# Kernel optimization log

Hardware: AMD Instinct MI355X
Metric: run time of the kernel (lower is better)

Reference implementation:

```python
import jax, jax.numpy as jnp
import numpy as np

EPS = 1e-6

def _rms_norm(x, w):
    # RMSNorm over last dim (head_dim)
    var = jnp.mean(jnp.square(x), axis=-1, keepdims=True)
    return x * jax.lax.rsqrt(var + EPS) * w

def _apply_rope(x, cos, sin):
    # x: [b, s, h, d]; cos/sin: [s, d]. Interleaved (real, imag) pairs as in
    # diffusers apply_rotary_emb (use_real_unbind_dim=-1) used by Flux.
    xr = x[..., 0::2]
    xi = x[..., 1::2]
    rotated = jnp.stack([-xi, xr], axis=-1).reshape(x.shape)
    cs = cos[None, :, None, :]
    sn = sin[None, :, None, :]
    return x * cs + rotated * sn

def setup_inputs() -> dict:
    key = jax.random.key(0)
    ks = jax.random.split(key, 10)
    b, s, dim, h, hd = 1, 2048, 3072, 24, 128
    inner = h * hd
    scale = 1.0 / np.sqrt(dim)
    x = jax.random.normal(ks[0], (b, s, dim), dtype=jnp.float32)
    # rope tables: proper cos/sin of log-spaced frequencies
    pos = jnp.arange(s, dtype=jnp.float32)[:, None]
    freqs = 1.0 / (10000.0 ** (jnp.arange(0, hd, 2, dtype=jnp.float32) / hd))
    angles = pos * freqs[None, :]                      # [s, hd/2]
    angles = jnp.repeat(angles, 2, axis=-1)            # [s, hd] interleaved pairs
    rope_cos = jnp.cos(angles)
    rope_sin = jnp.sin(angles)
    Wq = jax.random.normal(ks[1], (dim, inner), dtype=jnp.float32) * scale
    Wk = jax.random.normal(ks[2], (dim, inner), dtype=jnp.float32) * scale
    Wv = jax.random.normal(ks[3], (dim, inner), dtype=jnp.float32) * scale
    bq = jax.random.normal(ks[4], (inner,), dtype=jnp.float32) * 0.01
    bk = jax.random.normal(ks[5], (inner,), dtype=jnp.float32) * 0.01
    bv = jax.random.normal(ks[6], (inner,), dtype=jnp.float32) * 0.01
    gq = jnp.ones((hd,), dtype=jnp.float32)
    gk = jnp.ones((hd,), dtype=jnp.float32)
    return {"x": x, "rope_cos": rope_cos, "rope_sin": rope_sin,
            "Wq": Wq, "bq": bq, "Wk": Wk, "bk": bk, "Wv": Wv, "bv": bv,
            "gq": gq, "gk": gk}

def reference(x, rope_cos, rope_sin, Wq, bq, Wk, bk, Wv, bv, gq, gk):
    b, s, _ = x.shape
    h, hd = 24, 128
    q = (x @ Wq + bq).reshape(b, s, h, hd)
    k = (x @ Wk + bk).reshape(b, s, h, hd)
    v = (x @ Wv + bv).reshape(b, s, h, hd)
    q = _apply_rope(_rms_norm(q, gq), rope_cos, rope_sin)
    k = _apply_rope(_rms_norm(k, gk), rope_cos, rope_sin)
    scale = 1.0 / jnp.sqrt(jnp.asarray(hd, dtype=q.dtype))
    scores = jnp.einsum('bshd,bthd->bhst', q, k) * scale
    attn = jax.nn.softmax(scores, axis=-1)
    out = jnp.einsum('bhst,bthd->bshd', attn, v)
    return out.reshape(b, s, h * hd)
```

## Files before the change

kernel.cpp:

```cpp
#include <hip/hip_runtime.h>
#include <hip/hip_bf16.h>

typedef __attribute__((ext_vector_type(8))) short short8;
typedef __attribute__((ext_vector_type(4))) float f32x4;
typedef __attribute__((ext_vector_type(16))) float f32x16;

#define SEQ 2048
#define DIM 3072
#define NHEAD 24
#define HDIM 128
#define SCALE_Q 0.12751744f

__device__ __forceinline__ unsigned short f2bf(float f) {
  unsigned int b = __float_as_uint(f);
  b += 0x7fffu + ((b >> 16) & 1u);
  return (unsigned short)(b >> 16);
}
__device__ __forceinline__ float bf2f(unsigned short u) {
  return __uint_as_float(((unsigned int)u) << 16);
}
__device__ __forceinline__ unsigned int pkbf(float a, float b) {
  __hip_bfloat162 h = __float22bfloat162_rn(make_float2(a, b));
  return *(unsigned int*)&h;
}

__device__ __forceinline__ void async16(const void* g, void* l) {
  __builtin_amdgcn_global_load_lds(
      (const __attribute__((address_space(1))) unsigned int*)g,
      (__attribute__((address_space(3))) unsigned int*)l, 16, 0, 0);
}

__global__ void k_cvt_x(const float* __restrict__ x, unsigned short* __restrict__ xb) {
  int idx = (blockIdx.x * 256 + threadIdx.x) * 8;
  float4 a = *(const float4*)(x + idx);
  float4 b = *(const float4*)(x + idx + 4);
  short8 o;
  o[0] = (short)f2bf(a.x); o[1] = (short)f2bf(a.y);
  o[2] = (short)f2bf(a.z); o[3] = (short)f2bf(a.w);
  o[4] = (short)f2bf(b.x); o[5] = (short)f2bf(b.y);
  o[6] = (short)f2bf(b.z); o[7] = (short)f2bf(b.w);
  *(short8*)(xb + idx) = o;
}

__device__ __forceinline__ void transpose_tile(const float* __restrict__ w,
                                               unsigned short* __restrict__ wt,
                                               int n0, int k0, int outRowBase, int t) {
  __shared__ unsigned short tile[64][68];
  int c4 = (t & 15) * 4;
  int r0 = t >> 4;
#pragma unroll
  for (int j = 0; j < 4; ++j) {
    int r = r0 + 16 * j;
    float4 v = *(const float4*)(w + (size_t)(k0 + r) * DIM + n0 + c4);
    ushort4 u;
    u.x = f2bf(v.x); u.y = f2bf(v.y); u.z = f2bf(v.z); u.w = f2bf(v.w);
    *(ushort4*)&tile[r][c4] = u;
  }
  __syncthreads();
#pragma unroll
  for (int j = 0; j < 4; ++j) {
    int nn = r0 + 16 * j;
    ushort4 u;
    u.x = tile[c4 + 0][nn]; u.y = tile[c4 + 1][nn];
    u.z = tile[c4 + 2][nn]; u.w = tile[c4 + 3][nn];
    *(ushort4*)(wt + (size_t)(outRowBase + n0 + nn) * DIM + k0 + c4) = u;
  }
}

__global__ __launch_bounds__(256) void k_transpose(const float* __restrict__ w,
                                                   unsigned short* __restrict__ wt) {
  transpose_tile(w, wt, blockIdx.x * 64, blockIdx.y * 64, 0, threadIdx.x);
}

__global__ __launch_bounds__(256) void k_transpose3(const float* __restrict__ w0,
                                                    const float* __restrict__ w1,
                                                    const float* __restrict__ w2,
                                                    unsigned short* __restrict__ wt) {
  const float* w = blockIdx.z == 0 ? w0 : (blockIdx.z == 1 ? w1 : w2);
  transpose_tile(w, wt, blockIdx.x * 64, blockIdx.y * 64, blockIdx.z * DIM, threadIdx.x);
}

__device__ __forceinline__ void gemm_tile(const unsigned short* __restrict__ xb,
                                          const unsigned short* __restrict__ wt,
                                          int bm, int bn, int t, f32x4 (&acc)[4][4],
                                          unsigned short* As, unsigned short* Bs) {
  int l = t & 63, w = t >> 6;
  int wr = w >> 1, wc = w & 1;
  int lr = l & 15, kc = l >> 4;
  const char* aB = (const char*)xb;
  const char* bB = (const char*)wt;
  char* asmB = (char*)As;
  char* bsmB = (char*)Bs;
  int sw = (lr & 7) << 4;

  for (int k0 = 0; k0 < DIM; k0 += 64) {
#pragma unroll
    for (int i = 0; i < 4; ++i) {
      int off = (t + 256 * i) * 16;
      int row = off >> 7;
      int cb = off & 127;
      int scb = cb ^ ((row & 7) << 4);
      async16(aB + ((size_t)(bm * 128 + row) * DIM + k0) * 2 + scb, asmB + off);
      async16(bB + ((size_t)(bn * 128 + row) * DIM + k0) * 2 + scb, bsmB + off);
    }
    __syncthreads();
#pragma unroll
    for (int kk = 0; kk < 2; ++kk) {
      short8 af[4], bf[4];
#pragma unroll
      for (int m = 0; m < 4; ++m)
        af[m] = *(const short8*)(asmB + (wr * 64 + m * 16 + lr) * 128 +
                                 ((kk * 64 + kc * 16) ^ sw));
#pragma unroll
      for (int n = 0; n < 4; ++n)
        bf[n] = *(const short8*)(bsmB + (wc * 64 + n * 16 + lr) * 128 +
                                 ((kk * 64 + kc * 16) ^ sw));
#pragma unroll
      for (int m = 0; m < 4; ++m)
#pragma unroll
        for (int n = 0; n < 4; ++n)
          acc[m][n] = __builtin_amdgcn_mfma_f32_16x16x32_bf16(af[m], bf[n], acc[m][n], 0, 0, 0);
    }
    __syncthreads();
  }
}

__global__ __launch_bounds__(256) void k_gemm(const unsigned short* __restrict__ xb,
                                              const unsigned short* __restrict__ wt,
                                              const float* __restrict__ bias,
                                              unsigned short* __restrict__ out,
                                              int vmode) {
  __shared__ unsigned short As[128 * 64];
  __shared__ unsigned short Bs[128 * 64];
  int t = threadIdx.x;
  int fid = blockIdx.x;
  int logical = (fid & 7) * 48 + (fid >> 3);
  int bm = logical & 15, bn = logical >> 4;

  f32x4 acc[4][4];
#pragma unroll
  for (int m = 0; m < 4; ++m)
#pragma unroll
    for (int n = 0; n < 4; ++n) acc[m][n] = (f32x4){0.f, 0.f, 0.f, 0.f};

  gemm_tile(xb, wt, bm, bn, t, acc, As, Bs);

  int l = t & 63, w = t >> 6;
  int wr = w >> 1, wc = w & 1;
  int lr = l & 15, lq = l >> 4;
  if (vmode) {
#pragma unroll
    for (int m = 0; m < 4; ++m)
#pragma unroll
      for (int n = 0; n < 4; ++n) {
        int gcol = bn * 128 + wc * 64 + n * 16 + lr;
        float bv = bias[gcol];
        int grow = bm * 128 + wr * 64 + m * 16 + lq * 4;
        ushort4 u;
        u.x = f2bf(acc[m][n][0] + bv);
        u.y = f2bf(acc[m][n][1] + bv);
        u.z = f2bf(acc[m][n][2] + bv);
        u.w = f2bf(acc[m][n][3] + bv);
        *(ushort4*)(out + (size_t)gcol * SEQ + grow) = u;
      }
  } else {
#pragma unroll
    for (int m = 0; m < 4; ++m)
#pragma unroll
      for (int n = 0; n < 4; ++n) {
        int gcol = bn * 128 + wc * 64 + n * 16 + lr;
        float bv = bias[gcol];
#pragma unroll
        for (int i = 0; i < 4; ++i) {
          int grow = bm * 128 + wr * 64 + m * 16 + lq * 4 + i;
          out[(size_t)grow * DIM + gcol] = f2bf(acc[m][n][i] + bv);
        }
      }
  }
}

__global__ __launch_bounds__(256, 4) void k_gemm3(
    const unsigned short* __restrict__ xb, const unsigned short* __restrict__ wt,
    const float* __restrict__ bq, const float* __restrict__ bk,
    const float* __restrict__ bv, const float* __restrict__ rope_cos,
    const float* __restrict__ rope_sin, const float* __restrict__ gq,
    const float* __restrict__ gk, unsigned short* __restrict__ qb,
    unsigned short* __restrict__ kb, unsigned short* __restrict__ vtb) {
  __shared__ unsigned short As[128 * 64];
  __shared__ unsigned short Bs[128 * 64];
  __shared__ float ssum[2][128];
  int t = threadIdx.x;
  int fid = blockIdx.x;
  int xcd = fid & 7, li = fid >> 3;
  int c = li / 36, r = li % 36;
  int bnl9 = r >> 2, bmi = r & 3;
  int bm = c * 4 + bmi;
  int bn = xcd * 9 + bnl9;

  f32x4 acc[4][4];
#pragma unroll
  for (int m = 0; m < 4; ++m)
#pragma unroll
    for (int n = 0; n < 4; ++n) acc[m][n] = (f32x4){0.f, 0.f, 0.f, 0.f};

  gemm_tile(xb, wt, bm, bn, t, acc, As, Bs);

  int l = t & 63, w = t >> 6;
  int wr = w >> 1, wc = w & 1;
  int lr = l & 15, lq = l >> 4;

  int region = bn >= 48 ? 2 : (bn >= 24 ? 1 : 0);
  int bnl = bn - region * 24;
  const float* bias = region == 0 ? bq : (region == 1 ? bk : bv);

  if (region == 2) {
#pragma unroll
    for (int m = 0; m < 4; ++m)
#pragma unroll
      for (int n = 0; n < 4; ++n) {
        int gcol = bnl * 128 + wc * 64 + n * 16 + lr;
        float bv_ = bias[gcol];
        int grow = bm * 128 + wr * 64 + m * 16 + lq * 4;
        ushort4 u;
        u.x = f2bf(acc[m][n][0] + bv_);
        u.y = f2bf(acc[m][n][1] + bv_);
        u.z = f2bf(acc[m][n][2] + bv_);
        u.w = f2bf(acc[m][n][3] + bv_);
        *(ushort4*)(vtb + (size_t)gcol * SEQ + grow) = u;
      }
  } else {
    unsigned short* outp = region == 0 ? qb : kb;
    const float* g = region == 0 ? gq : gk;
    float scale = region == 0 ? SCALE_Q : 1.0f;

    float gv[4], bvv[4];
#pragma unroll
    for (int n = 0; n < 4; ++n) {
      int cl = wc * 64 + n * 16 + lr;
      gv[n] = g[cl];
      bvv[n] = bias[bnl * 128 + cl];
    }
#pragma unroll
    for (int m = 0; m < 4; ++m)
#pragma unroll
      for (int n = 0; n < 4; ++n)
#pragma unroll
        for (int i = 0; i < 4; ++i) acc[m][n][i] += bvv[n];

#pragma unroll
    for (int m = 0; m < 4; ++m)
#pragma unroll
      for (int i = 0; i < 4; ++i) {
        float ss = acc[m][0][i] * acc[m][0][i] + acc[m][1][i] * acc[m][1][i] +
                   acc[m][2][i] * acc[m][2][i] + acc[m][3][i] * acc[m][3][i];
        ss += __shfl_xor(ss, 1);
        ss += __shfl_xor(ss, 2);
        ss += __shfl_xor(ss, 4);
        ss += __shfl_xor(ss, 8);
        if (lr == m * 4 + i) ssum[wc][wr * 64 + m * 16 + lq * 4 + i] = ss;
      }
    __syncthreads();

#pragma unroll
    for (int m = 0; m < 4; ++m)
#pragma unroll
      for (int i = 0; i < 4; ++i) {
        int rl = wr * 64 + m * 16 + lq * 4 + i;
        float rn = rsqrtf((ssum[0][rl] + ssum[1][rl]) * (1.0f / 128.0f) + 1e-6f);
        int s_idx = bm * 128 + rl;
        const float* cr = rope_cos + (size_t)s_idx * HDIM;
        const float* sr = rope_sin + (size_t)s_idx * HDIM;
        unsigned short* orow = outp + (size_t)s_idx * DIM + bnl * 128;
#pragma unroll
        for (int n = 0; n < 4; ++n) {
          int cl = wc * 64 + n * 16 + lr;
          float xn = acc[m][n][i] * rn * gv[n];
          float pr = __shfl_xor(xn, 1);
          float cv = cr[cl], sv = sr[cl];
          float o = (lr & 1) ? fmaf(xn, cv, pr * sv) : fmaf(xn, cv, -pr * sv);
          orow[cl] = f2bf(o * scale);
        }
      }
  }
}

__global__ void k_normrope(unsigned short* __restrict__ qk, const float* __restrict__ cosb,
                           const float* __restrict__ sinb, const float* __restrict__ g,
                           float scale) {
  int t = threadIdx.x;
  int w = t >> 6, l = t & 63;
  int row = blockIdx.x * 4 + w;
  int s_idx = row / NHEAD, head = row % NHEAD;
  size_t base = (size_t)s_idx * DIM + head * HDIM;
  unsigned int pair = *(const unsigned int*)(qk + base + 2 * l);
  float x0 = bf2f((unsigned short)(pair & 0xffffu));
  float x1 = bf2f((unsigned short)(pair >> 16));
  float ss = x0 * x0 + x1 * x1;
#pragma unroll
  for (int off = 1; off < 64; off <<= 1) ss += __shfl_xor(ss, off);
  float r = rsqrtf(ss * (1.0f / 128.0f) + 1e-6f);
  float g0 = g[2 * l], g1 = g[2 * l + 1];
  float c0 = cosb[s_idx * HDIM + 2 * l], c1 = cosb[s_idx * HDIM + 2 * l + 1];
  float s0 = sinb[s_idx * HDIM + 2 * l], s1 = sinb[s_idx * HDIM + 2 * l + 1];
  float xn0 = x0 * r * g0, xn1 = x1 * r * g1;
  float o0 = (xn0 * c0 - xn1 * s0) * scale;
  float o1 = (xn1 * c1 + xn0 * s1) * scale;
  unsigned int po = (unsigned int)f2bf(o0) | ((unsigned int)f2bf(o1) << 16);
  *(unsigned int*)(qk + base + 2 * l) = po;
}

__global__ __launch_bounds__(256, 2) void k_attn(const unsigned short* __restrict__ q,
                                                 const unsigned short* __restrict__ k,
                                                 const unsigned short* __restrict__ vt,
                                                 float* __restrict__ out) {
  __shared__ unsigned short Ksm[2][64 * 128];
  __shared__ unsigned short Vtsm[2][128 * 64];
  int t = threadIdx.x;
  int w = t >> 6, l = t & 63;
  int q32 = l & 31, hi = l >> 5;
  int hi4 = hi * 4;
  int fid = blockIdx.x;
  int logical = (fid & 7) * 48 + (fid >> 3);
  int qt = logical & 15, h = logical >> 4;
  int q0w = qt * 128 + w * 32;

  const char* kbase = (const char*)k + (size_t)h * HDIM * 2;
  const char* vbase = (const char*)vt + (size_t)h * HDIM * SEQ * 2;

  int koff[4], voff[4], dst[4];
#pragma unroll
  for (int i = 0; i < 4; ++i) {
    int off = (t + 256 * i) * 16;
    dst[i] = off;
    int krow = off >> 8, kcb = off & 255;
    koff[i] = krow * (DIM * 2) + (kcb ^ ((krow & 15) << 4));
    int vrow = off >> 7, vcb = off & 127;
    voff[i] = vrow * (SEQ * 2) + (vcb ^ ((vrow & 7) << 4));
  }

  short8 qf[8];
  {
    const unsigned short* qrow = q + (size_t)(q0w + q32) * DIM + h * HDIM;
#pragma unroll
    for (int ks = 0; ks < 8; ++ks) qf[ks] = *(const short8*)(qrow + ks * 16 + hi * 8);
  }

  f32x16 o0 = {0.f,0.f,0.f,0.f,0.f,0.f,0.f,0.f,0.f,0.f,0.f,0.f,0.f,0.f,0.f,0.f};
  f32x16 o1 = o0, o2 = o0, o3 = o0;
  float m_ = -1e30f, lsum = 0.f;
  int ksw = (q32 & 15) << 4;
  int vsw = (q32 & 7) << 4;

  union U8 { short8 s8; unsigned int u[4]; };

#pragma unroll
  for (int i = 0; i < 4; ++i) {
    async16(kbase + koff[i], (char*)Ksm[0] + dst[i]);
    async16(vbase + voff[i], (char*)Vtsm[0] + dst[i]);
  }
  __syncthreads();

  for (int kt = 0; kt < 32; ++kt) {
    int cur = kt & 1;
    if (kt < 31) {
      const char* kt_k = kbase + (size_t)(kt + 1) * (64 * DIM * 2);
      const char* kt_v = vbase + (kt + 1) * 128;
#pragma unroll
      for (int i = 0; i < 4; ++i) {
        async16(kt_k + koff[i], (char*)Ksm[cur ^ 1] + dst[i]);
        async16(kt_v + voff[i], (char*)Vtsm[cur ^ 1] + dst[i]);
      }
    }

    f32x16 st0 = {0.f,0.f,0.f,0.f,0.f,0.f,0.f,0.f,0.f,0.f,0.f,0.f,0.f,0.f,0.f,0.f};
    f32x16 st1 = st0;
    {
      const char* kr0 = (const char*)Ksm[cur] + q32 * 256;
      const char* kr1 = (const char*)Ksm[cur] + (32 + q32) * 256;
      __builtin_amdgcn_s_setprio(1);
#pragma unroll
      for (int ks = 0; ks < 8; ++ks) {
        int cb = (ks * 32 + hi * 16) ^ ksw;
        short8 kf0 = *(const short8*)(kr0 + cb);
        short8 kf1 = *(const short8*)(kr1 + cb);
        st0 = __builtin_amdgcn_mfma_f32_32x32x16_bf16(kf0, qf[ks], st0, 0, 0, 0);
        st1 = __builtin_amdgcn_mfma_f32_32x32x16_bf16(kf1, qf[ks], st1, 0, 0, 0);
      }
      __builtin_amdgcn_s_setprio(0);
    }

    float mx = fmaxf(st0[0], st1[0]);
#pragma unroll
    for (int r = 1; r < 16; ++r) mx = fmaxf(mx, fmaxf(st0[r], st1[r]));
    mx = fmaxf(mx, __shfl_xor(mx, 32));

    if (__any(mx > m_ + 10.0f)) {
      float mn = fmaxf(m_, mx);
      float corr = exp2f(m_ - mn);
      m_ = mn;
      lsum *= corr;
#pragma unroll
      for (int r = 0; r < 16; ++r) {
        float cr = __shfl(corr, (r & 3) + 8 * (r >> 2) + hi4);
        o0[r] *= cr; o1[r] *= cr; o2[r] *= cr; o3[r] *= cr;
      }
    }

#pragma unroll
    for (int r = 0; r < 16; ++r) {
      st0[r] = exp2f(st0[r] - m_);
      st1[r] = exp2f(st1[r] - m_);
    }
    {
      float sm = st0[0] + st1[0];
#pragma unroll
      for (int r = 1; r < 16; ++r) sm += st0[r] + st1[r];
      sm += __shfl_xor(sm, 32);
      lsum += sm;
    }

    U8 pa[4];
#pragma unroll
    for (int b = 0; b < 4; ++b) {
      unsigned int a0, a1, a2, a3;
      if (b < 2) {
        int r0 = (b & 1) * 8;
        a0 = pkbf(st0[r0 + 0], st0[r0 + 1]);
        a1 = pkbf(st0[r0 + 2], st0[r0 + 3]);
        a2 = pkbf(st0[r0 + 4], st0[r0 + 5]);
        a3 = pkbf(st0[r0 + 6], st0[r0 + 7]);
      } else {
        int r0 = (b & 1) * 8;
        a0 = pkbf(st1[r0 + 0], st1[r0 + 1]);
        a1 = pkbf(st1[r0 + 2], st1[r0 + 3]);
        a2 = pkbf(st1[r0 + 4], st1[r0 + 5]);
        a3 = pkbf(st1[r0 + 6], st1[r0 + 7]);
      }
      asm volatile("v_permlane32_swap_b32 %0, %1" : "+v"(a0), "+v"(a2));
      asm volatile("v_permlane32_swap_b32 %0, %1" : "+v"(a1), "+v"(a3));
      pa[b].u[0] = a0; pa[b].u[1] = a1; pa[b].u[2] = a2; pa[b].u[3] = a3;
    }

    __builtin_amdgcn_s_setprio(1);
#pragma unroll
    for (int ks = 0; ks < 4; ++ks) {
      int cb = (ks * 32 + hi * 16) ^ vsw;
      const char* Vp = (const char*)Vtsm[cur];
      short8 vf0 = *(const short8*)(Vp + (0 * 32 + q32) * 128 + cb);
      short8 vf1 = *(const short8*)(Vp + (1 * 32 + q32) * 128 + cb);
      short8 vf2 = *(const short8*)(Vp + (2 * 32 + q32) * 128 + cb);
      short8 vf3 = *(const short8*)(Vp + (3 * 32 + q32) * 128 + cb);
      o0 = __builtin_amdgcn_mfma_f32_32x32x16_bf16(pa[ks].s8, vf0, o0, 0, 0, 0);
      o1 = __builtin_amdgcn_mfma_f32_32x32x16_bf16(pa[ks].s8, vf1, o1, 0, 0, 0);
      o2 = __builtin_amdgcn_mfma_f32_32x32x16_bf16(pa[ks].s8, vf2, o2, 0, 0, 0);
      o3 = __builtin_amdgcn_mfma_f32_32x32x16_bf16(pa[ks].s8, vf3, o3, 0, 0, 0);
    }
    __builtin_amdgcn_s_setprio(0);

    __syncthreads();
  }

  float inv = 1.0f / lsum;
#pragma unroll
  for (int r = 0; r < 16; ++r) {
    float fr = __shfl(inv, (r & 3) + 8 * (r >> 2) + hi4);
    int grow = q0w + (r & 3) + 8 * (r >> 2) + hi4;
    float* orow = out + (size_t)grow * DIM + h * HDIM + q32;
    orow[0]  = o0[r] * fr;
    orow[32] = o1[r] * fr;
    orow[64] = o2[r] * fr;
    orow[96] = o3[r] * fr;
  }
}

extern "C" void kernel_launch(void* const* d_in, const int* in_sizes, int n_in,
                              void* d_out, int out_size, void* d_ws, size_t ws_size,
                              hipStream_t stream) {
  const float* x = (const float*)d_in[0];
  const float* rope_cos = (const float*)d_in[1];
  const float* rope_sin = (const float*)d_in[2];
  const float* Wq = (const float*)d_in[3];
  const float* bq = (const float*)d_in[4];
  const float* Wk = (const float*)d_in[5];
  const float* bk = (const float*)d_in[6];
  const float* Wv = (const float*)d_in[7];
  const float* bv = (const float*)d_in[8];
  const float* gq = (const float*)d_in[9];
  const float* gk = (const float*)d_in[10];
  float* out = (float*)d_out;

  const size_t slab = (size_t)SEQ * DIM;
  const size_t wt9elems = (size_t)3 * DIM * DIM;
  const size_t need = (4 * slab + wt9elems) * 2;

  if (ws_size >= need) {
    unsigned short* xb = (unsigned short*)d_ws;
    unsigned short* wt9 = xb + slab;
    unsigned short* qb = wt9 + wt9elems;
    unsigned short* kb = qb + slab;
    unsigned short* vtb = kb + slab;

    k_cvt_x<<<3072, 256, 0, stream>>>(x, xb);
    k_transpose3<<<dim3(DIM / 64, DIM / 64, 3), 256, 0, stream>>>(Wq, Wk, Wv, wt9);
    k_gemm3<<<1152, 256, 0, stream>>>(xb, wt9, bq, bk, bv, rope_cos, rope_sin, gq, gk,
                                      qb, kb, vtb);
    k_attn<<<384, 256, 0, stream>>>(qb, kb, vtb, out);
  } else {
    unsigned short* xb = (unsigned short*)d_ws;
    unsigned short* wt = xb + slab;
    unsigned short* qb = wt + (size_t)DIM * DIM;
    unsigned short* kb = qb + slab;
    unsigned short* vtb = kb + slab;

    k_cvt_x<<<3072, 256, 0, stream>>>(x, xb);
    dim3 tg(DIM / 64, DIM / 64);
    k_transpose<<<tg, 256, 0, stream>>>(Wq, wt);
    k_gemm<<<384, 256, 0, stream>>>(xb, wt, bq, qb, 0);
    k_transpose<<<tg, 256, 0, stream>>>(Wk, wt);
    k_gemm<<<384, 256, 0, stream>>>(xb, wt, bk, kb, 0);
    k_transpose<<<tg, 256, 0, stream>>>(Wv, wt);
    k_gemm<<<384, 256, 0, stream>>>(xb, wt, bv, vtb, 1);
    k_normrope<<<SEQ * NHEAD / 4, 256, 0, stream>>>(qb, rope_cos, rope_sin, gq, SCALE_Q);
    k_normrope<<<SEQ * NHEAD / 4, 256, 0, stream>>>(kb, rope_cos, rope_sin, gk, 1.0f);
    k_attn<<<384, 256, 0, stream>>>(qb, kb, vtb, out);
  }
}
```

Before: 282.1 us.

## Rewrite fused QKV GEMM as 8-wave 128x256 tile with triple-buffered async loads

Replaces the 256-thread 128x128 QKV GEMM with a 512-thread kernel computing 128x256 tiles. K-slices of 32 are staged into three LDS buffers through async global-to-LDS copies with swizzled addressing, so loads overlap the MFMA work under priority hints. The norm/rope epilogue is adjusted so each tile covers two heads. The larger tile improves reuse, but the kernel runs half as many blocks and adds barriers on every K step.

```diff
diff --git a/kernel.cpp b/kernel.cpp
--- a/kernel.cpp
+++ b/kernel.cpp
@@ -179,23 +179,48 @@
   }
 }
 
-__global__ __launch_bounds__(256, 4) void k_gemm3(
+__global__ __launch_bounds__(512, 2) void k_gemm8(
     const unsigned short* __restrict__ xb, const unsigned short* __restrict__ wt,
     const float* __restrict__ bq, const float* __restrict__ bk,
     const float* __restrict__ bv, const float* __restrict__ rope_cos,
     const float* __restrict__ rope_sin, const float* __restrict__ gq,
     const float* __restrict__ gk, unsigned short* __restrict__ qb,
     unsigned short* __restrict__ kb, unsigned short* __restrict__ vtb) {
-  __shared__ unsigned short As[128 * 64];
-  __shared__ unsigned short Bs[128 * 64];
-  __shared__ float ssum[2][128];
-  int t = threadIdx.x;
+  __shared__ unsigned short As[3][128 * 32];
+  __shared__ unsigned short Bs[3][256 * 32];
+  __shared__ float ssum[4][128];
+  const int t = threadIdx.x;
+  const int l = t & 63, w = t >> 6;
+  const int wm = w >> 2, wn = w & 3;
+  const int lr = l & 15, lq = l >> 4;
   int fid = blockIdx.x;
-  int xcd = fid & 7, li = fid >> 3;
-  int c = li / 36, r = li % 36;
-  int bnl9 = r >> 2, bmi = r & 3;
-  int bm = c * 4 + bmi;
-  int bn = xcd * 9 + bnl9;
+  int g = (fid & 7) * 72 + (fid >> 3);
+  int bn = g >> 4, bm = g & 15;
+  const int sw3 = (lr & 3) << 4;
+
+  int adst, asrc;
+  {
+    int off = t * 16;
+    int row = off >> 6, cb = off & 63;
+    adst = off;
+    asrc = row * (DIM * 2) + (cb ^ ((row & 3) << 4));
+  }
+  int bdst0, bsrc0, bdst1, bsrc1;
+  {
+    int off = t * 16;
+    int row = off >> 6, cb = off & 63;
+    bdst0 = off;
+    bsrc0 = row * (DIM * 2) + (cb ^ ((row & 3) << 4));
+  }
+  {
+    int off = (t + 512) * 16;
+    int row = off >> 6, cb = off & 63;
+    bdst1 = off;
+    bsrc1 = row * (DIM * 2) + (cb ^ ((row & 3) << 4));
+  }
+
+  const char* aB = (const char*)xb + (size_t)bm * 128 * (DIM * 2);
+  const char* bB = (const char*)wt + (size_t)bn * 256 * (DIM * 2);
 
   f32x4 acc[4][4];
 #pragma unroll
@@ -203,49 +228,95 @@
 #pragma unroll
     for (int n = 0; n < 4; ++n) acc[m][n] = (f32x4){0.f, 0.f, 0.f, 0.f};
 
-  gemm_tile(xb, wt, bm, bn, t, acc, As, Bs);
-
-  int l = t & 63, w = t >> 6;
-  int wr = w >> 1, wc = w & 1;
-  int lr = l & 15, lq = l >> 4;
-
-  int region = bn >= 48 ? 2 : (bn >= 24 ? 1 : 0);
-  int bnl = bn - region * 24;
+  auto stage = [&](int kt, int b) {
+    int kcol = kt * 64;
+    async16(aB + asrc + kcol, (char*)As[b] + adst);
+    async16(bB + bsrc0 + kcol, (char*)Bs[b] + bdst0);
+    async16(bB + bsrc1 + kcol, (char*)Bs[b] + bdst1);
+  };
+
+  stage(0, 0);
+  stage(1, 1);
+  asm volatile("s_waitcnt vmcnt(3)");
+  __builtin_amdgcn_s_barrier();
+  __builtin_amdgcn_sched_barrier(0);
+
+  auto step = [&](int kt, int b, int bstage) {
+    short8 af[4], bf[4];
+    const char* Ab = (const char*)As[b];
+    const char* Bb = (const char*)Bs[b];
+    int colb = (lq * 16) ^ sw3;
+#pragma unroll
+    for (int mf = 0; mf < 4; ++mf)
+      af[mf] = *(const short8*)(Ab + (wm * 64 + mf * 16 + lr) * 64 + colb);
+#pragma unroll
+    for (int nf = 0; nf < 4; ++nf)
+      bf[nf] = *(const short8*)(Bb + (wn * 64 + nf * 16 + lr) * 64 + colb);
+    if (kt + 2 < 96) {
+      stage(kt + 2, bstage);
+      asm volatile("s_waitcnt vmcnt(3)");
+    } else {
+      asm volatile("s_waitcnt vmcnt(0)");
+    }
+    __builtin_amdgcn_s_barrier();
+    __builtin_amdgcn_sched_barrier(0);
+    __builtin_amdgcn_s_setprio(1);
+#pragma unroll
+    for (int mf = 0; mf < 4; ++mf)
+#pragma unroll
+      for (int nf = 0; nf < 4; ++nf)
+        acc[mf][nf] =
+            __builtin_amdgcn_mfma_f32_16x16x32_bf16(af[mf], bf[nf], acc[mf][nf], 0, 0, 0);
+    __builtin_amdgcn_s_setprio(0);
+    __builtin_amdgcn_s_barrier();
+    __builtin_amdgcn_sched_barrier(0);
+  };
+
+  for (int ko = 0; ko < 96; ko += 3) {
+    step(ko + 0, 0, 2);
+    step(ko + 1, 1, 0);
+    step(ko + 2, 2, 1);
+  }
+
+  int region = bn / 12;
+  int bnl = bn % 12;
   const float* bias = region == 0 ? bq : (region == 1 ? bk : bv);
 
   if (region == 2) {
 #pragma unroll
     for (int m = 0; m < 4; ++m)
 #pragma unroll
-      for (int n = 0; n < 4; ++n) {
-        int gcol = bnl * 128 + wc * 64 + n * 16 + lr;
+      for (int nf = 0; nf < 4; ++nf) {
+        int gcol = bnl * 256 + wn * 64 + nf * 16 + lr;
         float bv_ = bias[gcol];
-        int grow = bm * 128 + wr * 64 + m * 16 + lq * 4;
+        int grow = bm * 128 + wm * 64 + m * 16 + lq * 4;
         ushort4 u;
-        u.x = f2bf(acc[m][n][0] + bv_);
-        u.y = f2bf(acc[m][n][1] + bv_);
-        u.z = f2bf(acc[m][n][2] + bv_);
-        u.w = f2bf(acc[m][n][3] + bv_);
+        u.x = f2bf(acc[m][nf][0] + bv_);
+        u.y = f2bf(acc[m][nf][1] + bv_);
+        u.z = f2bf(acc[m][nf][2] + bv_);
+        u.w = f2bf(acc[m][nf][3] + bv_);
         *(ushort4*)(vtb + (size_t)gcol * SEQ + grow) = u;
       }
   } else {
     unsigned short* outp = region == 0 ? qb : kb;
-    const float* g = region == 0 ? gq : gk;
+    const float* gg = region == 0 ? gq : gk;
     float scale = region == 0 ? SCALE_Q : 1.0f;
+    int head = bnl * 2 + (wn >> 1);
 
     float gv[4], bvv[4];
-#pragma unroll
-    for (int n = 0; n < 4; ++n) {
-      int cl = wc * 64 + n * 16 + lr;
-      gv[n] = g[cl];
-      bvv[n] = bias[bnl * 128 + cl];
+    int colh[4];
+#pragma unroll
+    for (int nf = 0; nf < 4; ++nf) {
+      colh[nf] = (wn & 1) * 64 + nf * 16 + lr;
+      gv[nf] = gg[colh[nf]];
+      bvv[nf] = bias[head * 128 + colh[nf]];
     }
 #pragma unroll
     for (int m = 0; m < 4; ++m)
 #pragma unroll
-      for (int n = 0; n < 4; ++n)
-#pragma unroll
-        for (int i = 0; i < 4; ++i) acc[m][n][i] += bvv[n];
+      for (int nf = 0; nf < 4; ++nf)
+#pragma unroll
+        for (int i = 0; i < 4; ++i) acc[m][nf][i] += bvv[nf];
 
 #pragma unroll
     for (int m = 0; m < 4; ++m)
@@ -257,24 +328,25 @@
         ss += __shfl_xor(ss, 2);
         ss += __shfl_xor(ss, 4);
         ss += __shfl_xor(ss, 8);
-        if (lr == m * 4 + i) ssum[wc][wr * 64 + m * 16 + lq * 4 + i] = ss;
+        if (lr == m * 4 + i) ssum[wn][wm * 64 + m * 16 + lq * 4 + i] = ss;
       }
     __syncthreads();
 
+    int p = (wn >> 1) * 2;
 #pragma unroll
     for (int m = 0; m < 4; ++m)
 #pragma unroll
       for (int i = 0; i < 4; ++i) {
-        int rl = wr * 64 + m * 16 + lq * 4 + i;
-        float rn = rsqrtf((ssum[0][rl] + ssum[1][rl]) * (1.0f / 128.0f) + 1e-6f);
+        int rl = wm * 64 + m * 16 + lq * 4 + i;
+        float rn = rsqrtf((ssum[p][rl] + ssum[p + 1][rl]) * (1.0f / 128.0f) + 1e-6f);
         int s_idx = bm * 128 + rl;
         const float* cr = rope_cos + (size_t)s_idx * HDIM;
         const float* sr = rope_sin + (size_t)s_idx * HDIM;
-        unsigned short* orow = outp + (size_t)s_idx * DIM + bnl * 128;
-#pragma unroll
-        for (int n = 0; n < 4; ++n) {
-          int cl = wc * 64 + n * 16 + lr;
-          float xn = acc[m][n][i] * rn * gv[n];
+        unsigned short* orow = outp + (size_t)s_idx * DIM + head * 128;
+#pragma unroll
+        for (int nf = 0; nf < 4; ++nf) {
+          int cl = colh[nf];
+          float xn = acc[m][nf][i] * rn * gv[nf];
           float pr = __shfl_xor(xn, 1);
           float cv = cr[cl], sv = sr[cl];
           float o = (lr & 1) ? fmaf(xn, cv, pr * sv) : fmaf(xn, cv, -pr * sv);
@@ -502,8 +574,8 @@
 
     k_cvt_x<<<3072, 256, 0, stream>>>(x, xb);
     k_transpose3<<<dim3(DIM / 64, DIM / 64, 3), 256, 0, stream>>>(Wq, Wk, Wv, wt9);
-    k_gemm3<<<1152, 256, 0, stream>>>(xb, wt9, bq, bk, bv, rope_cos, rope_sin, gq, gk,
-                                      qb, kb, vtb);
+    k_gemm8<<<576, 512, 0, stream>>>(xb, wt9, bq, bk, bv, rope_cos, rope_sin, gq, gk,
+                                     qb, kb, vtb);
     k_attn<<<384, 256, 0, stream>>>(qb, kb, vtb, out);
   } else {
     unsigned short* xb = (unsigned short*)d_ws;
```

New measurement: 359.2 us. 27.3% more time.
